# Kernel optimization log

Hardware: AMD Instinct MI355X
Metric: run time of the kernel (lower is better)

Reference implementation:

```python
import jax, jax.numpy as jnp
import numpy as np

HEAD_DIM = 256
N_HEADS = 8
ROPE_BASE = 10000.0
EPS = 1e-6


def _rms(x):
    xf = x.astype(jnp.float32)
    return xf * jax.lax.rsqrt(jnp.mean(xf * xf, axis=-1, keepdims=True) + EPS)


def _rotate_half(x):
    x1, x2 = jnp.split(x, 2, axis=-1)
    return jnp.concatenate([-x2, x1], axis=-1)


def _mlp(h, wg, wu, wd):
    # Gemma gated MLP with gelu_pytorch_tanh activation
    return (jax.nn.gelu(h @ wg, approximate=True) * (h @ wu)) @ wd


def _qkv(h, wq, wk, wv):
    B, S, _ = h.shape
    q = (h @ wq).reshape(B, S, N_HEADS, HEAD_DIM).transpose(0, 2, 1, 3)  # [B,H,S,Dh]
    k = (h @ wk).reshape(B, S, HEAD_DIM)                                  # MQA: 1 kv head
    v = (h @ wv).reshape(B, S, HEAD_DIM)
    return q, k, v


def _forward(x_prefix, x_expert, attention_mask, adarms_cond, position_ids,
             p_ln1, p_wq, p_wk, p_wv, p_wo, p_ln2, p_wgate, p_wup, p_wdown,
             e_ada1_w, e_ada1_b, e_wq, e_wk, e_wv, e_wo, e_ada2_w, e_ada2_b,
             e_wgate, e_wup, e_wdown):
    B, S1, Dp = x_prefix.shape
    S2 = x_expert.shape[1]

    # --- pre-attention norms: plain Gemma RMSNorm (prefix), AdaRMS (expert) ---
    h_p = _rms(x_prefix) * (1.0 + p_ln1)
    mod1 = adarms_cond @ e_ada1_w + e_ada1_b                  # [B, 3*De]
    sc1, sh1, g1 = jnp.split(mod1, 3, axis=-1)
    h_e = _rms(x_expert) * (1.0 + sc1[:, None]) + sh1[:, None]
    gate1_e = g1[:, None]                                      # [B,1,De]

    # --- concatenated QKV across the two streams ---
    q_p, k_p, v_p = _qkv(h_p, p_wq, p_wk, p_wv)
    q_e, k_e, v_e = _qkv(h_e, e_wq, e_wk, e_wv)
    q = jnp.concatenate([q_p, q_e], axis=2)                    # [B,H,S,Dh]
    k = jnp.concatenate([k_p, k_e], axis=1)                    # [B,S,Dh]
    v = jnp.concatenate([v_p, v_e], axis=1)

    # --- rotary embedding on joint positions ---
    inv_freq = 1.0 / (ROPE_BASE ** (jnp.arange(0, HEAD_DIM, 2, dtype=jnp.float32) / HEAD_DIM))
    ang = position_ids.astype(jnp.float32)[..., None] * inv_freq
    emb = jnp.concatenate([ang, ang], axis=-1)                 # [B,S,Dh]
    cos, sin = jnp.cos(emb), jnp.sin(emb)
    q = q * cos[:, None] + _rotate_half(q) * sin[:, None]
    k = k * cos + _rotate_half(k) * sin

    # --- eager MQA attention ---
    scaling = HEAD_DIM ** -0.5
    scores = jnp.einsum('bhqd,bkd->bhqk', q, k) * scaling + attention_mask
    probs = jax.nn.softmax(scores.astype(jnp.float32), axis=-1)
    att = jnp.einsum('bhqk,bkd->bhqd', probs, v)
    att = att.transpose(0, 2, 1, 3).reshape(B, S1 + S2, N_HEADS * HEAD_DIM)

    # --- prefix stream: o_proj, residual, RMSNorm, gated MLP, residual ---
    res_p = x_prefix + att[:, :S1] @ p_wo
    h2_p = _rms(res_p) * (1.0 + p_ln2)
    out_p = res_p + _mlp(h2_p, p_wgate, p_wup, p_wdown)

    # --- expert stream: gated residuals from AdaRMS ---
    res_e = x_expert + gate1_e * (att[:, S1:] @ e_wo)
    mod2 = adarms_cond @ e_ada2_w + e_ada2_b
    sc2, sh2, g2 = jnp.split(mod2, 3, axis=-1)
    h2_e = _rms(res_e) * (1.0 + sc2[:, None]) + sh2[:, None]
    out_e = res_e + g2[:, None] * _mlp(h2_e, e_wgate, e_wup, e_wdown)
    return out_p, out_e


def setup_inputs() -> dict:
    key = jax.random.key(0)
    ks = iter(jax.random.split(key, 32))
    B, S1, S2 = 4, 768, 64
    Dp, De, Dh, H = 2048, 1024, 256, 8
    Fp, Fe = 16384, 4096

    def w(shape, s=0.02):
        return jax.random.normal(next(ks), shape, dtype=jnp.float32) * s

    return dict(
        x_prefix=jax.random.normal(next(ks), (B, S1, Dp), dtype=jnp.float32),
        x_expert=jax.random.normal(next(ks), (B, S2, De), dtype=jnp.float32),
        attention_mask=jnp.zeros((B, 1, S1 + S2, S1 + S2), dtype=jnp.float32),
        adarms_cond=jax.random.normal(next(ks), (B, De), dtype=jnp.float32),
        position_ids=jnp.sort(jax.random.randint(next(ks), (B, S1 + S2), 0, S1 + S2), axis=-1),
        p_ln1=jnp.zeros((Dp,), jnp.float32),
        p_wq=w((Dp, H * Dh)), p_wk=w((Dp, Dh)), p_wv=w((Dp, Dh)), p_wo=w((H * Dh, Dp)),
        p_ln2=jnp.zeros((Dp,), jnp.float32),
        p_wgate=w((Dp, Fp)), p_wup=w((Dp, Fp)), p_wdown=w((Fp, Dp)),
        e_ada1_w=w((De, 3 * De)), e_ada1_b=jnp.zeros((3 * De,), jnp.float32),
        e_wq=w((De, H * Dh)), e_wk=w((De, Dh)), e_wv=w((De, Dh)), e_wo=w((H * Dh, De)),
        e_ada2_w=w((De, 3 * De)), e_ada2_b=jnp.zeros((3 * De,), jnp.float32),
        e_wgate=w((De, Fe)), e_wup=w((De, Fe)), e_wdown=w((Fe, De)),
    )


def reference(x_prefix, x_expert, attention_mask, adarms_cond, position_ids,
              p_ln1, p_wq, p_wk, p_wv, p_wo, p_ln2, p_wgate, p_wup, p_wdown,
              e_ada1_w, e_ada1_b, e_wq, e_wk, e_wv, e_wo, e_ada2_w, e_ada2_b,
              e_wgate, e_wup, e_wdown):
    return _forward(x_prefix, x_expert, attention_mask, adarms_cond, position_ids,
                    p_ln1, p_wq, p_wk, p_wv, p_wo, p_ln2, p_wgate, p_wup, p_wdown,
                    e_ada1_w, e_ada1_b, e_wq, e_wk, e_wv, e_wo, e_ada2_w, e_ada2_b,
                    e_wgate, e_wup, e_wdown)
```

## Files before the change

kernel.cpp:

```cpp
#include <hip/hip_runtime.h>
#include <stdint.h>

typedef unsigned short ushort_t;
typedef __attribute__((ext_vector_type(8))) short short8;
typedef __attribute__((ext_vector_type(4))) float f32x4;

#define DEVINL __device__ __forceinline__

DEVINL ushort_t f2bf(float f){
  union { float f; uint32_t u; } v; v.f = f;
  uint32_t u = v.u;
  uint32_t r = (u + 0x7fffu + ((u >> 16) & 1u)) >> 16;
  return (ushort_t)r;
}
DEVINL float bf2f(ushort_t h){
  union { uint32_t u; float f; } v; v.u = ((uint32_t)h) << 16;
  return v.f;
}
DEVINL f32x4 mfma16(short8 a, short8 b, f32x4 c){
  return __builtin_amdgcn_mfma_f32_16x16x32_bf16(a, b, c, 0, 0, 0);
}
DEVINL void gload_lds16(const void* g, void* l){
  __builtin_amdgcn_global_load_lds((const __attribute__((address_space(1))) void*)g,
                                   (__attribute__((address_space(3))) void*)l, 16, 0, 0);
}
DEVINL float gelu_tanh(float x){
  return 0.5f * x * (1.f + tanhf(0.7978845608028654f * (x + 0.044715f * x * x * x)));
}

#define BAR() __builtin_amdgcn_s_barrier()
#define LGK0() asm volatile("s_waitcnt lgkmcnt(0)" ::: "memory")
#define VMC4() asm volatile("s_waitcnt vmcnt(4)" ::: "memory")
#define VMC0() asm volatile("s_waitcnt vmcnt(0)" ::: "memory")
#define PRIO1() __builtin_amdgcn_s_setprio(1)
#define PRIO0() __builtin_amdgcn_s_setprio(0)

__global__ void transpose_bf16(const float* __restrict__ W, ushort_t* __restrict__ Wt,
                               int K, int N)
{
  __shared__ ushort_t tile[64 * 65];
  const int t = threadIdx.x;
  const int k0 = blockIdx.y * 64, n0 = blockIdx.x * 64;
#pragma unroll
  for (int rr = 0; rr < 4; ++rr){
    const int row = rr * 16 + (t >> 4);
    const int c4 = (t & 15) * 4;
    float4 v = *(const float4*)&W[(size_t)(k0 + row) * N + n0 + c4];
    ushort_t* dst = &tile[row * 65 + c4];
    dst[0] = f2bf(v.x); dst[1] = f2bf(v.y); dst[2] = f2bf(v.z); dst[3] = f2bf(v.w);
  }
  __syncthreads();
  const int n = t >> 2, kc = (t & 3) * 16;
  __align__(16) ushort_t tmp[16];
#pragma unroll
  for (int j = 0; j < 16; ++j) tmp[j] = tile[(kc + j) * 65 + n];
  ushort_t* out = &Wt[(size_t)(n0 + n) * K + k0 + kc];
  *(short8*)&out[0] = *(short8*)&tmp[0];
  *(short8*)&out[8] = *(short8*)&tmp[8];
}

__global__ void mod_kernel(const float* __restrict__ cond,
                           const float* __restrict__ w1, const float* __restrict__ b1,
                           const float* __restrict__ w2, const float* __restrict__ b2,
                           float* __restrict__ mod1, float* __restrict__ mod2)
{
  __shared__ float cs[1024];
  const int bid = blockIdx.x, tid = threadIdx.x;
  const int which = bid / 48, rem = bid % 48, b = rem / 12, j0 = (rem % 12) * 256;
  const float* W = which ? w2 : w1;
  const float* bias = which ? b2 : b1;
  float* out = which ? mod2 : mod1;
#pragma unroll
  for (int i = 0; i < 4; ++i) cs[i * 256 + tid] = cond[b * 1024 + i * 256 + tid];
  __syncthreads();
  const int j = j0 + tid;
  float acc = bias[j];
  for (int k = 0; k < 1024; ++k) acc = fmaf(cs[k], W[(size_t)k * 3072 + j], acc);
  out[b * 3072 + j] = acc;
}

__global__ void rms_kernel(const float* __restrict__ x, ushort_t* __restrict__ out, int D,
                           const float* __restrict__ sw, const float* __restrict__ sh,
                           int mod_rpb, int mod_stride)
{
  const int row = blockIdx.x, tid = threadIdx.x;
  const float* xr = x + (size_t)row * D;
  const int nc = D >> 10;
  float ss = 0.f;
  for (int c = 0; c < nc; ++c){
    float4 v = *(const float4*)&xr[c * 1024 + tid * 4];
    ss += v.x * v.x + v.y * v.y + v.z * v.z + v.w * v.w;
  }
  for (int o = 32; o > 0; o >>= 1) ss += __shfl_xor(ss, o);
  __shared__ float red[4];
  if ((tid & 63) == 0) red[tid >> 6] = ss;
  __syncthreads();
  const float scale = rsqrtf((red[0] + red[1] + red[2] + red[3]) / (float)D + 1e-6f);
  const float* swp = sw;
  const float* shp = sh;
  if (mod_rpb){
    int bb = row / mod_rpb;
    swp += (size_t)bb * mod_stride;
    if (shp) shp += (size_t)bb * mod_stride;
  }
  for (int c = 0; c < nc; ++c){
    const int d = c * 1024 + tid * 4;
    float4 v = *(const float4*)&xr[d];
    float vv[4] = {v.x, v.y, v.z, v.w};
#pragma unroll
    for (int i = 0; i < 4; ++i){
      float tv = vv[i] * scale * (1.f + swp[d + i]);
      if (shp) tv += shp[d + i];
      out[(size_t)row * D + d + i] = f2bf(tv);
    }
  }
}

__global__ void rope_kernel(const ushort_t* __restrict__ qkv_p, const ushort_t* __restrict__ qkv_e,
                            const int* __restrict__ pos_ids,
                            ushort_t* __restrict__ q_all, ushort_t* __restrict__ k_all,
                            ushort_t* __restrict__ vT)
{
  const int tok = blockIdx.x, tid = threadIdx.x;
  int b, s;
  const ushort_t* src;
  if (tok < 3072){ b = tok / 768; s = tok - b * 768; src = qkv_p + (size_t)tok * 2560; }
  else { int te = tok - 3072; b = te >> 6; s = 768 + (te & 63); src = qkv_e + (size_t)te * 2560; }
  const int pos = pos_ids[b * 832 + s];
  __shared__ float cs[128], sn[128];
  if (tid < 128){
    float f = powf(10000.f, -(float)tid * (1.f / 128.f));
    float a = (float)pos * f;
    cs[tid] = cosf(a); sn[tid] = sinf(a);
  }
  __syncthreads();
#pragma unroll
  for (int c = 0; c < 10; ++c){
    const int n = c * 256 + tid;
    const float v = bf2f(src[n]);
    if (n < 2048){
      const int h = n >> 8, d = n & 255;
      const float o = bf2f(src[(h << 8) + ((d < 128) ? (d + 128) : (d - 128))]);
      const int dd = d & 127;
      const float r = (d < 128) ? v * cs[dd] - o * sn[dd] : v * cs[dd] + o * sn[dd];
      q_all[(((size_t)(b * 8 + h)) * 832 + s) * 256 + d] = f2bf(r);
    } else if (n < 2304){
      const int d = n - 2048;
      const float o = bf2f(src[2048 + ((d < 128) ? (d + 128) : (d - 128))]);
      const int dd = d & 127;
      const float r = (d < 128) ? v * cs[dd] - o * sn[dd] : v * cs[dd] + o * sn[dd];
      k_all[((size_t)(b * 832) + s) * 256 + d] = f2bf(r);
    } else {
      const int d = n - 2304;
      vT[((size_t)(b * 256) + d) * 832 + s] = src[n];
    }
  }
}

__global__ void __launch_bounds__(256, 2)
attn_kernel(const ushort_t* __restrict__ q_all, const ushort_t* __restrict__ k_all,
            const ushort_t* __restrict__ vT, const float* __restrict__ mask,
            ushort_t* __restrict__ att)
{
  __shared__ __align__(16) ushort_t Ks[64 * 256];
  __shared__ __align__(16) ushort_t Vs[256 * 64];
  __shared__ __align__(16) ushort_t Ps[4][16 * 72];
  const int tid = threadIdx.x, lane = tid & 63, wid = tid >> 6;
  const int l15 = lane & 15, lg = lane >> 4;
  const int qt = blockIdx.x, h = blockIdx.y, b = blockIdx.z;
  const int q0 = qt * 64 + wid * 16;

  short8 qf[8];
  {
    const ushort_t* qr = q_all + (((size_t)(b * 8 + h) * 832) + q0 + l15) * 256;
#pragma unroll
    for (int s = 0; s < 8; ++s) qf[s] = *(const short8*)&qr[s * 32 + lg * 8];
  }

  f32x4 accO[16] = {};
  float mrow[4] = {-3.0e38f, -3.0e38f, -3.0e38f, -3.0e38f};
  float lrow[4] = {0.f, 0.f, 0.f, 0.f};

  for (int kt = 0; kt < 13; ++kt){
    const int s0 = kt * 64;
#pragma unroll
    for (int i = 0; i < 8; ++i){
      const int o = i * 256 + tid;
      gload_lds16(k_all + ((size_t)(b * 832) + s0 + (o >> 5)) * 256 + (o & 31) * 8, &Ks[o * 8]);
      gload_lds16(vT + ((size_t)(b * 256) + (o >> 3)) * 832 + s0 + (o & 7) * 8, &Vs[o * 8]);
    }
    __syncthreads();

    f32x4 sc[4] = {};
#pragma unroll
    for (int s = 0; s < 8; ++s){
#pragma unroll
      for (int nf = 0; nf < 4; ++nf){
        short8 kb = *(const short8*)&Ks[(nf * 16 + l15) * 256 + s * 32 + lg * 8];
        sc[nf] = mfma16(qf[s], kb, sc[nf]);
      }
    }
#pragma unroll
    for (int nf = 0; nf < 4; ++nf){
#pragma unroll
      for (int r = 0; r < 4; ++r){
        const int q = q0 + lg * 4 + r;
        const int kk = s0 + nf * 16 + l15;
        sc[nf][r] = sc[nf][r] * 0.0625f + mask[((size_t)b * 832 + q) * 832 + kk];
      }
    }
    float al[4];
#pragma unroll
    for (int r = 0; r < 4; ++r){
      float tm = fmaxf(fmaxf(sc[0][r], sc[1][r]), fmaxf(sc[2][r], sc[3][r]));
      tm = fmaxf(tm, __shfl_xor(tm, 1));
      tm = fmaxf(tm, __shfl_xor(tm, 2));
      tm = fmaxf(tm, __shfl_xor(tm, 4));
      tm = fmaxf(tm, __shfl_xor(tm, 8));
      const float mnew = fmaxf(mrow[r], tm);
      al[r] = __expf(mrow[r] - mnew);
      mrow[r] = mnew;
      float rs = 0.f;
#pragma unroll
      for (int nf = 0; nf < 4; ++nf){
        const float p = __expf(sc[nf][r] - mnew);
        rs += p;
        Ps[wid][(lg * 4 + r) * 72 + nf * 16 + l15] = f2bf(p);
      }
      rs += __shfl_xor(rs, 1);
      rs += __shfl_xor(rs, 2);
      rs += __shfl_xor(rs, 4);
      rs += __shfl_xor(rs, 8);
      lrow[r] = lrow[r] * al[r] + rs;
    }
#pragma unroll
    for (int nd = 0; nd < 16; ++nd){
#pragma unroll
      for (int r = 0; r < 4; ++r) accO[nd][r] *= al[r];
    }
#pragma unroll
    for (int ks = 0; ks < 2; ++ks){
      short8 pa = *(const short8*)&Ps[wid][l15 * 72 + ks * 32 + lg * 8];
#pragma unroll
      for (int nd = 0; nd < 16; ++nd){
        short8 vb = *(const short8*)&Vs[(nd * 16 + l15) * 64 + ks * 32 + lg * 8];
        accO[nd] = mfma16(pa, vb, accO[nd]);
      }
    }
    __syncthreads();
  }
#pragma unroll
  for (int nd = 0; nd < 16; ++nd){
#pragma unroll
    for (int r = 0; r < 4; ++r){
      const int q = q0 + lg * 4 + r;
      const int d = nd * 16 + l15;
      att[((size_t)(b * 832) + q) * 2048 + h * 256 + d] = f2bf(accO[nd][r] / lrow[r]);
    }
  }
}

template<int EPI>
__global__ void __launch_bounds__(256, 2)
gemm_bt(const ushort_t* __restrict__ A, int lda, int a_rpb, int a_bstride, int a_r0,
        const ushort_t* __restrict__ Bt, int ldb,
        void* __restrict__ Cv, int N, int K,
        const void* __restrict__ Xv,
        const float* __restrict__ gatep, int gate_stride, int gate_rpb,
        size_t pstride)
{
  __shared__ __align__(16) ushort_t As[128 * 64];
  __shared__ __align__(16) ushort_t Bs[128 * 64];
  const int tid = threadIdx.x;
  const int lane = tid & 63;
  const int l15 = lane & 15, lg = lane >> 4;
  const int wid = tid >> 6;
  const int wm = (wid >> 1) * 64, wn = (wid & 1) * 64;
  const int m0 = blockIdx.y * 128, n0 = blockIdx.x * 128;
  const int z = blockIdx.z;
  const int kbeg = z * K, kend = z * K + K;

  size_t abase[4], bbase[4];
  const int k8 = (tid & 7) * 8;
#pragma unroll
  for (int i = 0; i < 4; ++i){
    const int row = (i * 256 + tid) >> 3;
    const int r = m0 + row;
    const int bb = r / a_rpb;
    const int arow = bb * a_bstride + a_r0 + (r - bb * a_rpb);
    abase[i] = (size_t)arow * lda + k8;
    bbase[i] = (size_t)(n0 + row) * ldb + k8;
  }

  f32x4 acc[4][4] = {};

  for (int kt = kbeg; kt < kend; kt += 64){
#pragma unroll
    for (int i = 0; i < 4; ++i){
      gload_lds16(A + abase[i] + kt, &As[(i * 256 + tid) * 8]);
      gload_lds16(Bt + bbase[i] + kt, &Bs[(i * 256 + tid) * 8]);
    }
    __syncthreads();
#pragma unroll
    for (int s = 0; s < 2; ++s){
      const int ko = s * 32 + lg * 8;
      short8 af[4], bfr[4];
#pragma unroll
      for (int i = 0; i < 4; ++i) af[i] = *(const short8*)&As[(wm + i * 16 + l15) * 64 + ko];
#pragma unroll
      for (int j = 0; j < 4; ++j) bfr[j] = *(const short8*)&Bs[(wn + j * 16 + l15) * 64 + ko];
#pragma unroll
      for (int i = 0; i < 4; ++i)
#pragma unroll
        for (int j = 0; j < 4; ++j)
          acc[i][j] = mfma16(af[i], bfr[j], acc[i][j]);
    }
    __syncthreads();
  }

#pragma unroll
  for (int i = 0; i < 4; ++i){
#pragma unroll
    for (int r = 0; r < 4; ++r){
      const int m = m0 + wm + i * 16 + lg * 4 + r;
#pragma unroll
      for (int j = 0; j < 4; ++j){
        const int n = n0 + wn + j * 16 + l15;
        const size_t idx = (size_t)m * N + n;
        const float v = acc[i][j][r];
        if (EPI == 0){
          ((ushort_t*)Cv)[idx] = f2bf(v);
        } else if (EPI == 1){
          const float g = bf2f(((const ushort_t*)Xv)[idx]);
          ((ushort_t*)Cv)[idx] = f2bf(gelu_tanh(g) * v);
        } else if (EPI == 2){
          ((float*)Cv)[idx] = ((const float*)Xv)[idx] + v;
        } else if (EPI == 3){
          const int bb = m / gate_rpb;
          ((float*)Cv)[idx] = ((const float*)Xv)[idx] + gatep[(size_t)bb * gate_stride + n] * v;
        } else {
          ((float*)Cv)[(size_t)z * pstride + idx] = v;
        }
      }
    }
  }
}

#define MMAQ(AF, BF, MQ, NQ) \
  { _Pragma("unroll") for (int i_ = 0; i_ < 4; ++i_){ \
      _Pragma("unroll") for (int j_ = 0; j_ < 2; ++j_){ \
        _Pragma("unroll") for (int s_ = 0; s_ < 2; ++s_){ \
          acc[(MQ)*4 + i_][(NQ)*2 + j_] = \
            mfma16(AF[i_][s_], BF[j_][s_], acc[(MQ)*4 + i_][(NQ)*2 + j_]); } } } }

template<int EPI>
__global__ void __launch_bounds__(512, 1)
gemm8(const ushort_t* __restrict__ A, int lda,
      const ushort_t* __restrict__ Bt, int ldb,
      void* __restrict__ Cv, int N, int klen,
      const void* __restrict__ Xv, size_t pstride)
{
  __shared__ __align__(16) ushort_t As[2][256 * 64];
  __shared__ __align__(16) ushort_t Bs[2][256 * 64];

  const int tid = threadIdx.x;
  const int lane = tid & 63, wid = tid >> 6;
  const int l15 = lane & 15, lg = lane >> 4;
  const int wm = (wid >> 2) * 128, wn = (wid & 3) * 64;

  const int gx = gridDim.x, nwg = gx * gridDim.y;
  const int orig = blockIdx.y * gx + blockIdx.x;
  const int q = nwg >> 3, r = nwg & 7;
  const int xcd = orig & 7, lo = orig >> 3;
  const int wg = (xcd < r ? xcd * (q + 1) : r * (q + 1) + (xcd - r) * q) + lo;
  const int m0 = (wg / gx) * 256, n0 = (wg % gx) * 256;
  const int z = blockIdx.z;
  const size_t k0 = (size_t)z * klen;
  const int NT = klen >> 6;

  auto stage = [&](int buf, int half, int kt){
    const ushort_t* src; int ld, r0; ushort_t* dst;
    if (half < 2){ src = A;  ld = lda; r0 = m0 + half * 128; dst = &As[buf][half * 8192]; }
    else         { src = Bt; ld = ldb; r0 = n0 + (half - 2) * 128; dst = &Bs[buf][(half - 2) * 8192]; }
#pragma unroll
    for (int c = 0; c < 2; ++c){
      const int idx = c * 512 + tid;
      const int row = idx >> 3, slot = idx & 7;
      gload_lds16(src + (size_t)(r0 + row) * ld + k0 + kt + ((slot ^ (row & 7)) << 3),
                  dst + idx * 8);
    }
  };
  auto readA = [&](short8 (&f)[4][2], int buf, int mq){
#pragma unroll
    for (int i = 0; i < 4; ++i){
      const int row = wm + mq * 64 + i * 16 + l15;
#pragma unroll
      for (int s = 0; s < 2; ++s)
        f[i][s] = *(const short8*)&As[buf][row * 64 + (((s * 4 + lg) ^ (row & 7)) << 3)];
    }
  };
  auto readB = [&](short8 (&f)[2][2], int buf, int nq){
#pragma unroll
    for (int j = 0; j < 2; ++j){
      const int row = wn + nq * 32 + j * 16 + l15;
#pragma unroll
      for (int s = 0; s < 2; ++s)
        f[j][s] = *(const short8*)&Bs[buf][row * 64 + (((s * 4 + lg) ^ (row & 7)) << 3)];
    }
  };

  stage(0, 0, 0); stage(0, 1, 0); stage(0, 2, 0); stage(0, 3, 0);
  if (NT > 1){ stage(1, 2, 64); stage(1, 0, 64); VMC4(); } else { VMC0(); }
  BAR();

  short8 af[4][2], bq0[2][2], bq1[2][2];
  f32x4 acc[8][4] = {};

  for (int t = 0; t < NT; ++t){
    const int cur = t & 1, nxt = cur ^ 1;
    const int kc1 = (t + 1) << 6, kc2 = (t + 2) << 6;
    readA(af, cur, 0);
    readB(bq0, cur, 0);
    if (t + 1 < NT) stage(nxt, 1, kc1);
    BAR(); LGK0();
    PRIO1(); MMAQ(af, bq0, 0, 0); PRIO0(); BAR();
    readB(bq1, cur, 1);
    if (t + 1 < NT) stage(nxt, 3, kc1);
    BAR(); LGK0();
    PRIO1(); MMAQ(af, bq1, 0, 1); PRIO0(); BAR();
    readA(af, cur, 1);
    if (t + 2 < NT) stage(cur, 2, kc2);
    BAR(); LGK0();
    PRIO1(); MMAQ(af, bq1, 1, 1); PRIO0(); BAR();
    if (t + 2 < NT){ stage(cur, 0, kc2); VMC4(); } else { VMC0(); }
    BAR();
    PRIO1(); MMAQ(af, bq0, 1, 0); PRIO0(); BAR();
  }

#pragma unroll
  for (int i = 0; i < 8; ++i){
#pragma unroll
    for (int rr = 0; rr < 4; ++rr){
      const int m = m0 + wm + i * 16 + lg * 4 + rr;
#pragma unroll
      for (int j = 0; j < 4; ++j){
        const int n = n0 + wn + j * 16 + l15;
        const size_t idx = (size_t)m * N + n;
        const float v = acc[i][j][rr];
        if (EPI == 0){
          ((ushort_t*)Cv)[idx] = f2bf(v);
        } else if (EPI == 1){
          const float g = bf2f(((const ushort_t*)Xv)[idx]);
          ((ushort_t*)Cv)[idx] = f2bf(gelu_tanh(g) * v);
        } else {
          ((float*)Cv)[(size_t)z * pstride + idx] = v;
        }
      }
    }
  }
}

__global__ void reduce4(const float* __restrict__ part, const float* __restrict__ res,
                        float* __restrict__ out, int total4, size_t pstride)
{
  int i = blockIdx.x * blockDim.x + threadIdx.x;
  const int stride = gridDim.x * blockDim.x;
  for (; i < total4; i += stride){
    const size_t e = (size_t)i * 4;
    float4 a = *(const float4*)&res[e];
#pragma unroll
    for (int z = 0; z < 4; ++z){
      float4 p = *(const float4*)&part[(size_t)z * pstride + e];
      a.x += p.x; a.y += p.y; a.z += p.z; a.w += p.w;
    }
    *(float4*)&out[e] = a;
  }
}

__global__ void fuse_gelu(const float* __restrict__ pg, const float* __restrict__ pu,
                          ushort_t* __restrict__ out, int total4, size_t pstride)
{
  int i = blockIdx.x * blockDim.x + threadIdx.x;
  const int stride = gridDim.x * blockDim.x;
  for (; i < total4; i += stride){
    const size_t e = (size_t)i * 4;
    float4 g = *(const float4*)&pg[e];
    float4 u = *(const float4*)&pu[e];
#pragma unroll
    for (int z = 1; z < 4; ++z){
      float4 a = *(const float4*)&pg[(size_t)z * pstride + e];
      float4 b = *(const float4*)&pu[(size_t)z * pstride + e];
      g.x += a.x; g.y += a.y; g.z += a.z; g.w += a.w;
      u.x += b.x; u.y += b.y; u.z += b.z; u.w += b.w;
    }
    out[e + 0] = f2bf(gelu_tanh(g.x) * u.x);
    out[e + 1] = f2bf(gelu_tanh(g.y) * u.y);
    out[e + 2] = f2bf(gelu_tanh(g.z) * u.z);
    out[e + 3] = f2bf(gelu_tanh(g.w) * u.w);
  }
}

__global__ void reduce_gated(const float* __restrict__ part, size_t pstride, int nz,
                             const float* __restrict__ base, const float* __restrict__ gate,
                             int gstride, int rpb, int N,
                             float* __restrict__ out, int total4)
{
  int i = blockIdx.x * blockDim.x + threadIdx.x;
  const int stride = gridDim.x * blockDim.x;
  for (; i < total4; i += stride){
    const size_t e = (size_t)i * 4;
    const int row = (int)(e / N), n = (int)(e % N);
    const int b = row / rpb;
    float4 s = *(const float4*)&part[e];
    for (int z = 1; z < nz; ++z){
      float4 p = *(const float4*)&part[(size_t)z * pstride + e];
      s.x += p.x; s.y += p.y; s.z += p.z; s.w += p.w;
    }
    float4 bs = *(const float4*)&base[e];
    const float* gp = &gate[(size_t)b * gstride + n];
    bs.x += gp[0] * s.x; bs.y += gp[1] * s.y; bs.z += gp[2] * s.z; bs.w += gp[3] * s.w;
    *(float4*)&out[e] = bs;
  }
}

extern "C" void kernel_launch(void* const* d_in, const int* in_sizes, int n_in,
                              void* d_out, int out_size, void* d_ws, size_t ws_size,
                              hipStream_t stream)
{
  const float* x_prefix = (const float*)d_in[0];
  const float* x_expert = (const float*)d_in[1];
  const float* mask     = (const float*)d_in[2];
  const float* cond     = (const float*)d_in[3];
  const int*   pos      = (const int*)d_in[4];
  const float* p_ln1    = (const float*)d_in[5];
  const float* p_wq     = (const float*)d_in[6];
  const float* p_wk     = (const float*)d_in[7];
  const float* p_wv     = (const float*)d_in[8];
  const float* p_wo     = (const float*)d_in[9];
  const float* p_ln2    = (const float*)d_in[10];
  const float* p_wgate  = (const float*)d_in[11];
  const float* p_wup    = (const float*)d_in[12];
  const float* p_wdown  = (const float*)d_in[13];
  const float* e_ada1_w = (const float*)d_in[14];
  const float* e_ada1_b = (const float*)d_in[15];
  const float* e_wq     = (const float*)d_in[16];
  const float* e_wk     = (const float*)d_in[17];
  const float* e_wv     = (const float*)d_in[18];
  const float* e_wo     = (const float*)d_in[19];
  const float* e_ada2_w = (const float*)d_in[20];
  const float* e_ada2_b = (const float*)d_in[21];
  const float* e_wgate  = (const float*)d_in[22];
  const float* e_wup    = (const float*)d_in[23];
  const float* e_wdown  = (const float*)d_in[24];

  char* ws = (char*)d_ws;
  size_t off = 0;
  auto alloc = [&](size_t bytes) -> char* {
    char* p = ws + off;
    off += bytes;
    off = (off + 255) & ~(size_t)255;
    return p;
  };

  ushort_t* t_wqkv_p  = (ushort_t*)alloc((size_t)2560 * 2048 * 2);
  ushort_t* t_wo_p    = (ushort_t*)alloc((size_t)2048 * 2048 * 2);
  ushort_t* t_wgate_p = (ushort_t*)alloc((size_t)16384 * 2048 * 2);
  ushort_t* t_wup_p   = (ushort_t*)alloc((size_t)16384 * 2048 * 2);
  ushort_t* t_wdown_p = (ushort_t*)alloc((size_t)2048 * 16384 * 2);
  ushort_t* t_wqkv_e  = (ushort_t*)alloc((size_t)2560 * 1024 * 2);
  ushort_t* t_wo_e    = (ushort_t*)alloc((size_t)1024 * 2048 * 2);
  ushort_t* t_wgate_e = (ushort_t*)alloc((size_t)4096 * 1024 * 2);
  ushort_t* t_wup_e   = (ushort_t*)alloc((size_t)4096 * 1024 * 2);
  ushort_t* t_wdown_e = (ushort_t*)alloc((size_t)1024 * 4096 * 2);
  float* mod1 = (float*)alloc((size_t)4 * 3072 * 4);
  float* mod2 = (float*)alloc((size_t)4 * 3072 * 4);
  float* res_p = (float*)alloc((size_t)3072 * 2048 * 4);
  float* res_e = (float*)alloc((size_t)256 * 1024 * 4);
  ushort_t* h2_p = (ushort_t*)alloc((size_t)3072 * 2048 * 2);
  ushort_t* h2_e = (ushort_t*)alloc((size_t)256 * 1024 * 2);
  ushort_t* g_e  = (ushort_t*)alloc((size_t)256 * 4096 * 2);

  const size_t zone_off = off;
  ushort_t* h_p   = (ushort_t*)alloc((size_t)3072 * 2048 * 2);
  ushort_t* h_e   = (ushort_t*)alloc((size_t)256 * 1024 * 2);
  ushort_t* qkv_p = (ushort_t*)alloc((size_t)3072 * 2560 * 2);
  ushort_t* qkv_e = (ushort_t*)alloc((size_t)256 * 2560 * 2);
  ushort_t* q_all = (ushort_t*)alloc((size_t)4 * 8 * 832 * 256 * 2);
  ushort_t* k_all = (ushort_t*)alloc((size_t)4 * 832 * 256 * 2);
  ushort_t* vTb   = (ushort_t*)alloc((size_t)4 * 256 * 832 * 2);
  ushort_t* att   = (ushort_t*)alloc((size_t)4 * 832 * 2048 * 2);
  const size_t phase1_end = off;
  ushort_t* g_p = (ushort_t*)(ws + zone_off);

  float* partials = (float*)t_wgate_p;
  const size_t PSTRIDE_P = (size_t)3072 * 2048;
  float* pwo = (float*)(ws + zone_off);
  const size_t PSTRIDE_E = (size_t)256 * 1024;
  float* pg = (float*)t_wgate_p;
  float* pu = pg + (size_t)4 * 256 * 4096;
  float* pd = pu + (size_t)4 * 256 * 4096;
  const size_t PSTRIDE_GE = (size_t)256 * 4096;

  const size_t g_p_end = zone_off + (size_t)3072 * 16384 * 2;
  const size_t needed = (phase1_end > g_p_end) ? phase1_end : g_p_end;
  if (ws_size < needed) return;

  const int BIG = 1 << 30;

  transpose_bf16<<<dim3(2048/64, 2048/64), 256, 0, stream>>>(p_wq, t_wqkv_p, 2048, 2048);
  transpose_bf16<<<dim3(256/64, 2048/64), 256, 0, stream>>>(p_wk, t_wqkv_p + (size_t)2048*2048, 2048, 256);
  transpose_bf16<<<dim3(256/64, 2048/64), 256, 0, stream>>>(p_wv, t_wqkv_p + (size_t)2304*2048, 2048, 256);
  transpose_bf16<<<dim3(2048/64, 2048/64), 256, 0, stream>>>(p_wo, t_wo_p, 2048, 2048);
  transpose_bf16<<<dim3(16384/64, 2048/64), 256, 0, stream>>>(p_wgate, t_wgate_p, 2048, 16384);
  transpose_bf16<<<dim3(16384/64, 2048/64), 256, 0, stream>>>(p_wup, t_wup_p, 2048, 16384);
  transpose_bf16<<<dim3(2048/64, 16384/64), 256, 0, stream>>>(p_wdown, t_wdown_p, 16384, 2048);
  transpose_bf16<<<dim3(2048/64, 1024/64), 256, 0, stream>>>(e_wq, t_wqkv_e, 1024, 2048);
  transpose_bf16<<<dim3(256/64, 1024/64), 256, 0, stream>>>(e_wk, t_wqkv_e + (size_t)2048*1024, 1024, 256);
  transpose_bf16<<<dim3(256/64, 1024/64), 256, 0, stream>>>(e_wv, t_wqkv_e + (size_t)2304*1024, 1024, 256);
  transpose_bf16<<<dim3(1024/64, 2048/64), 256, 0, stream>>>(e_wo, t_wo_e, 2048, 1024);
  transpose_bf16<<<dim3(4096/64, 1024/64), 256, 0, stream>>>(e_wgate, t_wgate_e, 1024, 4096);
  transpose_bf16<<<dim3(4096/64, 1024/64), 256, 0, stream>>>(e_wup, t_wup_e, 1024, 4096);
  transpose_bf16<<<dim3(1024/64, 4096/64), 256, 0, stream>>>(e_wdown, t_wdown_e, 4096, 1024);

  mod_kernel<<<96, 256, 0, stream>>>(cond, e_ada1_w, e_ada1_b, e_ada2_w, e_ada2_b, mod1, mod2);

  rms_kernel<<<3072, 256, 0, stream>>>(x_prefix, h_p, 2048, p_ln1, nullptr, 0, 0);
  rms_kernel<<<256, 256, 0, stream>>>(x_expert, h_e, 1024, mod1, mod1 + 1024, 64, 3072);

  gemm_bt<0><<<dim3(20, 24), 256, 0, stream>>>(h_p, 2048, BIG, 0, 0, t_wqkv_p, 2048,
                                               qkv_p, 2560, 2048, nullptr, nullptr, 0, 1, 0);
  gemm_bt<0><<<dim3(20, 2), 256, 0, stream>>>(h_e, 1024, BIG, 0, 0, t_wqkv_e, 1024,
                                              qkv_e, 2560, 1024, nullptr, nullptr, 0, 1, 0);

  rope_kernel<<<3328, 256, 0, stream>>>(qkv_p, qkv_e, pos, q_all, k_all, vTb);

  attn_kernel<<<dim3(13, 8, 4), 256, 0, stream>>>(q_all, k_all, vTb, mask, att);

  gemm_bt<2><<<dim3(16, 24), 256, 0, stream>>>(att, 2048, 768, 832, 0, t_wo_p, 2048,
                                               res_p, 2048, 2048, x_prefix, nullptr, 0, 1, 0);
  gemm_bt<4><<<dim3(8, 2, 4), 256, 0, stream>>>(att, 2048, 64, 832, 768, t_wo_e, 2048,
                                                pwo, 1024, 512, nullptr, nullptr, 0, 1, PSTRIDE_E);
  reduce_gated<<<256, 256, 0, stream>>>(pwo, PSTRIDE_E, 4, x_expert, mod1 + 2048, 3072, 64, 1024,
                                        res_e, (256 * 1024) / 4);

  rms_kernel<<<3072, 256, 0, stream>>>(res_p, h2_p, 2048, p_ln2, nullptr, 0, 0);
  rms_kernel<<<256, 256, 0, stream>>>(res_e, h2_e, 1024, mod2, mod2 + 1024, 64, 3072);

  gemm8<0><<<dim3(64, 12, 1), 512, 0, stream>>>(h2_p, 2048, t_wgate_p, 2048,
                                                g_p, 16384, 2048, nullptr, 0);
  gemm8<1><<<dim3(64, 12, 1), 512, 0, stream>>>(h2_p, 2048, t_wup_p, 2048,
                                                g_p, 16384, 2048, g_p, 0);
  gemm8<4><<<dim3(8, 12, 4), 512, 0, stream>>>(g_p, 16384, t_wdown_p, 16384,
                                               partials, 2048, 4096, nullptr, PSTRIDE_P);
  reduce4<<<2048, 256, 0, stream>>>(partials, res_p, (float*)d_out,
                                    (3072 * 2048) / 4, PSTRIDE_P);

  gemm_bt<4><<<dim3(32, 2, 4), 256, 0, stream>>>(h2_e, 1024, BIG, 0, 0, t_wgate_e, 1024,
                                                 pg, 4096, 256, nullptr, nullptr, 0, 1, PSTRIDE_GE);
  gemm_bt<4><<<dim3(32, 2, 4), 256, 0, stream>>>(h2_e, 1024, BIG, 0, 0, t_wup_e, 1024,
                                                 pu, 4096, 256, nullptr, nullptr, 0, 1, PSTRIDE_GE);
  fuse_gelu<<<1024, 256, 0, stream>>>(pg, pu, g_e, (256 * 4096) / 4, PSTRIDE_GE);
  gemm_bt<4><<<dim3(8, 2, 8), 256, 0, stream>>>(g_e, 4096, BIG, 0, 0, t_wdown_e, 4096,
                                                pd, 1024, 512, nullptr, nullptr, 0, 1, PSTRIDE_E);
  reduce_gated<<<256, 256, 0, stream>>>(pd, PSTRIDE_E, 8, res_e, mod2 + 2048, 3072, 64, 1024,
                                        (float*)d_out + (size_t)3072 * 2048, (256 * 1024) / 4);
}
```

Before: 1.393 ms.

## Collapse GEMM main loop into two phases and precompute LDS/global addresses

Measured after the change: 1.308 ms. 6.1% less time.

```diff
diff --git a/kernel.cpp b/kernel.cpp
--- a/kernel.cpp
+++ b/kernel.cpp
@@ -353,6 +353,16 @@
           acc[(MQ)*4 + i_][(NQ)*2 + j_] = \
             mfma16(AF[i_][s_], BF[j_][s_], acc[(MQ)*4 + i_][(NQ)*2 + j_]); } } } }
 
+#define READA(F, BUF, OA) \
+  { _Pragma("unroll") for (int i_ = 0; i_ < 4; ++i_){ \
+      _Pragma("unroll") for (int s_ = 0; s_ < 2; ++s_){ \
+        F[i_][s_] = *(const short8*)&(BUF)[OA[i_][s_]]; } } }
+
+#define READB(F, BUF, OB) \
+  { _Pragma("unroll") for (int j_ = 0; j_ < 2; ++j_){ \
+      _Pragma("unroll") for (int s_ = 0; s_ < 2; ++s_){ \
+        F[j_][s_] = *(const short8*)&(BUF)[OB[j_][s_]]; } } }
+
 template<int EPI>
 __global__ void __launch_bounds__(512, 1)
 gemm8(const ushort_t* __restrict__ A, int lda,
@@ -378,39 +388,51 @@
   const size_t k0 = (size_t)z * klen;
   const int NT = klen >> 6;
 
+  uint32_t offA0[4][2], offA1[4][2], offB0[2][2], offB1[2][2];
+#pragma unroll
+  for (int i = 0; i < 4; ++i){
+#pragma unroll
+    for (int s = 0; s < 2; ++s){
+      int r0 = wm + 0 * 64 + i * 16 + l15;
+      int r1 = wm + 1 * 64 + i * 16 + l15;
+      offA0[i][s] = r0 * 64 + (((s * 4 + lg) ^ (r0 & 7)) << 3);
+      offA1[i][s] = r1 * 64 + (((s * 4 + lg) ^ (r1 & 7)) << 3);
+    }
+  }
+#pragma unroll
+  for (int j = 0; j < 2; ++j){
+#pragma unroll
+    for (int s = 0; s < 2; ++s){
+      int r0 = wn + 0 * 32 + j * 16 + l15;
+      int r1 = wn + 1 * 32 + j * 16 + l15;
+      offB0[j][s] = r0 * 64 + (((s * 4 + lg) ^ (r0 & 7)) << 3);
+      offB1[j][s] = r1 * 64 + (((s * 4 + lg) ^ (r1 & 7)) << 3);
+    }
+  }
+
+  const ushort_t* gptr[4][2];
+  uint32_t ldso[2];
+#pragma unroll
+  for (int c = 0; c < 2; ++c){
+    const int idx = c * 512 + tid;
+    const int row = idx >> 3, slot = idx & 7;
+    const uint32_t sw = (uint32_t)((slot ^ (row & 7)) << 3);
+    ldso[c] = (uint32_t)idx * 8;
+    gptr[0][c] = A  + (size_t)(m0 + row) * lda + k0 + sw;
+    gptr[1][c] = A  + (size_t)(m0 + 128 + row) * lda + k0 + sw;
+    gptr[2][c] = Bt + (size_t)(n0 + row) * ldb + k0 + sw;
+    gptr[3][c] = Bt + (size_t)(n0 + 128 + row) * ldb + k0 + sw;
+  }
+
   auto stage = [&](int buf, int half, int kt){
-    const ushort_t* src; int ld, r0; ushort_t* dst;
-    if (half < 2){ src = A;  ld = lda; r0 = m0 + half * 128; dst = &As[buf][half * 8192]; }
-    else         { src = Bt; ld = ldb; r0 = n0 + (half - 2) * 128; dst = &Bs[buf][(half - 2) * 8192]; }
-#pragma unroll
-    for (int c = 0; c < 2; ++c){
-      const int idx = c * 512 + tid;
-      const int row = idx >> 3, slot = idx & 7;
-      gload_lds16(src + (size_t)(r0 + row) * ld + k0 + kt + ((slot ^ (row & 7)) << 3),
-                  dst + idx * 8);
-    }
+    ushort_t* base = (half < 2) ? &As[buf][(half & 1) * 8192] : &Bs[buf][(half & 1) * 8192];
+#pragma unroll
+    for (int c = 0; c < 2; ++c)
+      gload_lds16(gptr[half][c] + kt, base + ldso[c]);
   };
-  auto readA = [&](short8 (&f)[4][2], int buf, int mq){
-#pragma unroll
-    for (int i = 0; i < 4; ++i){
-      const int row = wm + mq * 64 + i * 16 + l15;
-#pragma unroll
-      for (int s = 0; s < 2; ++s)
-        f[i][s] = *(const short8*)&As[buf][row * 64 + (((s * 4 + lg) ^ (row & 7)) << 3)];
-    }
-  };
-  auto readB = [&](short8 (&f)[2][2], int buf, int nq){
-#pragma unroll
-    for (int j = 0; j < 2; ++j){
-      const int row = wn + nq * 32 + j * 16 + l15;
-#pragma unroll
-      for (int s = 0; s < 2; ++s)
-        f[j][s] = *(const short8*)&Bs[buf][row * 64 + (((s * 4 + lg) ^ (row & 7)) << 3)];
-    }
-  };
 
   stage(0, 0, 0); stage(0, 1, 0); stage(0, 2, 0); stage(0, 3, 0);
-  if (NT > 1){ stage(1, 2, 64); stage(1, 0, 64); VMC4(); } else { VMC0(); }
+  if (NT > 1){ stage(1, 2, 64); stage(1, 3, 64); VMC4(); } else { VMC0(); }
   BAR();
 
   short8 af[4][2], bq0[2][2], bq1[2][2];
@@ -419,22 +441,18 @@
   for (int t = 0; t < NT; ++t){
     const int cur = t & 1, nxt = cur ^ 1;
     const int kc1 = (t + 1) << 6, kc2 = (t + 2) << 6;
-    readA(af, cur, 0);
-    readB(bq0, cur, 0);
-    if (t + 1 < NT) stage(nxt, 1, kc1);
+    const ushort_t* Ac = As[cur];
+    const ushort_t* Bc = Bs[cur];
+    READA(af, Ac, offA0);
+    READB(bq0, Bc, offB0);
+    READB(bq1, Bc, offB1);
+    if (t + 1 < NT){ stage(nxt, 0, kc1); stage(nxt, 1, kc1); }
     BAR(); LGK0();
-    PRIO1(); MMAQ(af, bq0, 0, 0); PRIO0(); BAR();
-    readB(bq1, cur, 1);
-    if (t + 1 < NT) stage(nxt, 3, kc1);
+    PRIO1(); MMAQ(af, bq0, 0, 0); MMAQ(af, bq1, 0, 1); PRIO0(); BAR();
+    READA(af, Ac, offA1);
+    if (t + 2 < NT){ stage(cur, 2, kc2); stage(cur, 3, kc2); VMC4(); } else { VMC0(); }
     BAR(); LGK0();
-    PRIO1(); MMAQ(af, bq1, 0, 1); PRIO0(); BAR();
-    readA(af, cur, 1);
-    if (t + 2 < NT) stage(cur, 2, kc2);
-    BAR(); LGK0();
-    PRIO1(); MMAQ(af, bq1, 1, 1); PRIO0(); BAR();
-    if (t + 2 < NT){ stage(cur, 0, kc2); VMC4(); } else { VMC0(); }
-    BAR();
-    PRIO1(); MMAQ(af, bq0, 1, 0); PRIO0(); BAR();
+    PRIO1(); MMAQ(af, bq1, 1, 1); MMAQ(af, bq0, 1, 0); PRIO0(); BAR();
   }
 
 #pragma unroll
```
